# Optimization experiments

Hardware: AMD Instinct MI355X
Metric: run time of the kernel (lower is better)

## Reference

```python
import jax, jax.numpy as jnp
import numpy as np

B, I, T = 8192, 128, 21
H1, H2, H3 = 256, 256, 128


def _init(key, shape, fan_in):
    # torch-style uniform(-1/sqrt(fan_in), 1/sqrt(fan_in))
    bound = 1.0 / np.sqrt(fan_in)
    return jax.random.uniform(key, shape, jnp.float32, -bound, bound)


def setup_inputs() -> dict:
    key = jax.random.key(0)
    ks = jax.random.split(key, 16)
    x = jax.random.normal(ks[0], (B, I, T), jnp.float32)
    d = {"x": x}
    # stacked LSTM weights (PyTorch layout: W_ih (4H, in), gate order i,f,g,o)
    d["W1_ih"] = _init(ks[1], (4 * H1, I), H1)
    d["b1_ih"] = _init(ks[2], (4 * H1,), H1)
    d["b1_hh"] = _init(ks[3], (4 * H1,), H1)
    d["W2_ih"] = _init(ks[4], (4 * H2, H1), H2)
    d["b2_ih"] = _init(ks[5], (4 * H2,), H2)
    d["b2_hh"] = _init(ks[6], (4 * H2,), H2)
    d["W3_ih"] = _init(ks[7], (4 * H3, H2), H3)
    d["b3_ih"] = _init(ks[8], (4 * H3,), H3)
    d["b3_hh"] = _init(ks[9], (4 * H3,), H3)
    d["fc1_w"] = _init(ks[10], (1, H3), H3)
    d["fc1_b"] = _init(ks[11], (1,), H3)
    d["fc2_w"] = _init(ks[12], (T, T), T)
    d["fc2_b"] = _init(ks[13], (T,), T)
    return d


def _lstm_cell_step(xt, W_ih, b_ih, b_hh):
    # single timestep with h0 = c0 = 0, so the W_hh @ h0 term vanishes
    gates = xt @ W_ih.T + (b_ih + b_hh)          # (B, 21, 4H)
    i, f, g, o = jnp.split(gates, 4, axis=-1)    # torch gate order i,f,g,o
    c = jax.nn.sigmoid(i) * jnp.tanh(g)          # f * c0 = 0
    return jax.nn.sigmoid(o) * jnp.tanh(c)


def reference(x, W1_ih, b1_ih, b1_hh, W2_ih, b2_ih, b2_hh,
              W3_ih, b3_ih, b3_hh, fc1_w, fc1_b, fc2_w, fc2_b):
    # fold the 21 independent single-step columns into the batch dim
    xt = jnp.transpose(x, (0, 2, 1))             # (B, 21, I)
    h1 = _lstm_cell_step(xt, W1_ih, b1_ih, b1_hh)   # (B, 21, H1)
    h2 = _lstm_cell_step(h1, W2_ih, b2_ih, b2_hh)   # (B, 21, H2)
    h3 = _lstm_cell_step(h2, W3_ih, b3_ih, b3_hh)   # (B, 21, H3)
    y = h3 @ fc1_w.T + fc1_b                     # (B, 21, 1)
    y = y[..., 0][:, None, :]                    # (B, 1, 21)  == x_torch
    out = y @ fc2_w.T + fc2_b                    # (B, 1, 21)
    return out
```

## Files before the change

### kernel.cpp

```cpp
#include <hip/hip_runtime.h>
#include <hip/hip_bf16.h>
#include <stdint.h>


typedef __attribute__((ext_vector_type(8))) short bf16x8;
typedef __attribute__((ext_vector_type(4))) float f32x4;

#define M_ROWS 172032
#define BATCH  8192

__device__ __forceinline__ float bf2f(unsigned short u) {
    union { unsigned int i; float f; } v; v.i = ((unsigned int)u) << 16; return v.f;
}
__device__ __forceinline__ unsigned short f2bf(float f) {
    union { float f; unsigned int i; } v; v.f = f;
    unsigned int r = v.i + 0x7fffu + ((v.i >> 16) & 1u);
    return (unsigned short)(r >> 16);
}

#define LOG2E  1.44269504f
#define LOG2E2 2.88539008f

__device__ __forceinline__ float lstm_h(float gi, float gg, float go) {
    gg = fminf(fmaxf(gg, -15.0f), 15.0f);
    float Eg = __builtin_amdgcn_exp2f(gg * LOG2E2);
    float Ei = __builtin_amdgcn_exp2f(-gi * LOG2E);
    float c  = (Eg - 1.0f) * __builtin_amdgcn_rcpf((Eg + 1.0f) * (1.0f + Ei));
    float Eo = __builtin_amdgcn_exp2f(-go * LOG2E);
    float c2 = c * c;
    float num = c * fmaf(c2, c2 + 105.0f, 945.0f);
    float den = fmaf(c2, fmaf(15.0f, c2, 420.0f), 945.0f);
    return num * __builtin_amdgcn_rcpf(den * (1.0f + Eo));
}

__device__ __forceinline__ void gload_lds16(const unsigned short* g, unsigned short* l) {
    __builtin_amdgcn_global_load_lds(
        (const __attribute__((address_space(1))) unsigned int*)g,
        (__attribute__((address_space(3))) unsigned int*)l,
        16, 0, 0);
}

__global__ __launch_bounds__(256) void k_convert(
    const float* __restrict__ src, unsigned short* __restrict__ dst, int n4)
{
    int i = blockIdx.x * 256 + threadIdx.x;
    if (i < n4) {
        float4 v = ((const float4*)src)[i];
        ushort4 o;
        o.x = f2bf(v.x); o.y = f2bf(v.y); o.z = f2bf(v.z); o.w = f2bf(v.w);
        ((ushort4*)dst)[i] = o;
    }
}

__global__ __launch_bounds__(256) void k_transpose(
    const float* __restrict__ x, unsigned short* __restrict__ xt)
{
    __shared__ unsigned short tile[128 * 22];
    const int b = blockIdx.x, tid = threadIdx.x;
    const float* xb = x + (size_t)b * 2688;
    for (int idx = tid; idx < 2688; idx += 256) {
        int i = idx / 21, t = idx - i * 21;
        tile[i * 22 + t] = f2bf(xb[idx]);
    }
    __syncthreads();
    unsigned short* xtb = xt + (size_t)b * 2688;
    for (int idx = tid; idx < 2688; idx += 256) {
        int t = idx >> 7, i = idx & 127;
        xtb[t * 128 + i] = tile[i * 22 + t];
    }
}

template<int K, int HG>
__global__ __launch_bounds__(256, 2) void k_gemm_act(
    const unsigned short* __restrict__ A,
    const unsigned short* __restrict__ W,
    const float* __restrict__ bih,
    const float* __restrict__ bhh,
    unsigned short* __restrict__ Hout)
{
    __shared__ __align__(16) unsigned short As[128 * 64];
    __shared__ __align__(16) unsigned short Ws[192 * 64];

    const int tid  = threadIdx.x;
    const int wave = tid >> 6;
    const int lane = tid & 63;
    const int wm = wave >> 1;
    const int wn = wave & 1;
    const int r0 = blockIdx.x * 128;
    const int c0 = blockIdx.y * 64;
    const int csel = lane & 15;

    const unsigned short* aptr[4];
#pragma unroll
    for (int i = 0; i < 4; ++i) {
        int q16 = (wave * 4 + i) * 64 + lane;
        int row = q16 >> 3, pslot = q16 & 7;
        int lslot = pslot ^ (row & 7);
        aptr[i] = A + (size_t)(r0 + row) * K + lslot * 8;
    }
    const unsigned short* wptr[6];
#pragma unroll
    for (int i = 0; i < 6; ++i) {
        int q16 = (wave * 6 + i) * 64 + lane;
        int lrow = q16 >> 3, pslot = q16 & 7;
        int lslot = pslot ^ (lrow & 7);
        int gate = lrow >> 6, n = lrow & 63;
        int gbase = (gate == 0) ? 0 : (gate + 1) * HG;
        wptr[i] = W + (size_t)(gbase + c0 + n) * K + lslot * 8;
    }

    float bias[3][2];
#pragma unroll
    for (int n = 0; n < 2; ++n) {
        int cloc = c0 + wn * 32 + n * 16 + csel;
        bias[0][n] = bih[cloc] + bhh[cloc];
        bias[1][n] = bih[2 * HG + cloc] + bhh[2 * HG + cloc];
        bias[2][n] = bih[3 * HG + cloc] + bhh[3 * HG + cloc];
    }

    f32x4 acc[3][4][2];
#pragma unroll
    for (int g = 0; g < 3; ++g)
#pragma unroll
        for (int m = 0; m < 4; ++m)
#pragma unroll
            for (int n = 0; n < 2; ++n)
                acc[g][m][n] = (f32x4){0.f, 0.f, 0.f, 0.f};

#pragma unroll
    for (int kk = 0; kk < K; kk += 64) {
        if (kk) __syncthreads();
#pragma unroll
        for (int i = 0; i < 4; ++i)
            gload_lds16(aptr[i] + kk, &As[(wave * 4 + i) * 512]);
#pragma unroll
        for (int i = 0; i < 6; ++i)
            gload_lds16(wptr[i] + kk, &Ws[(wave * 6 + i) * 512]);
        __syncthreads();

#pragma unroll
        for (int ks = 0; ks < 64; ks += 32) {
            bf16x8 af[4];
            bf16x8 bfr[3][2];
            const int rsel = lane & 15;
            const int slot = (ks >> 3) | (lane >> 4);
            const int soff = (slot ^ (rsel & 7)) * 8;
#pragma unroll
            for (int m = 0; m < 4; ++m)
                af[m] = *(const bf16x8*)&As[(wm * 64 + m * 16 + rsel) * 64 + soff];
#pragma unroll
            for (int g = 0; g < 3; ++g)
#pragma unroll
                for (int n = 0; n < 2; ++n)
                    bfr[g][n] = *(const bf16x8*)&Ws[(g * 64 + wn * 32 + n * 16 + rsel) * 64 + soff];
#pragma unroll
            for (int g = 0; g < 3; ++g)
#pragma unroll
                for (int m = 0; m < 4; ++m)
#pragma unroll
                    for (int n = 0; n < 2; ++n)
                        acc[g][m][n] = __builtin_amdgcn_mfma_f32_16x16x32_bf16(
                            af[m], bfr[g][n], acc[g][m][n], 0, 0, 0);
        }
    }

    const int quad = lane >> 4;
#pragma unroll
    for (int m = 0; m < 4; ++m) {
#pragma unroll
        for (int n = 0; n < 2; ++n) {
            int cloc = wn * 32 + n * 16 + csel;
            f32x4 vi = acc[0][m][n], vg = acc[1][m][n], vo = acc[2][m][n];
#pragma unroll
            for (int r = 0; r < 4; ++r) {
                int row = r0 + wm * 64 + m * 16 + quad * 4 + r;
                float h = lstm_h(vi[r] + bias[0][n], vg[r] + bias[1][n],
                                 vo[r] + bias[2][n]);
                Hout[(size_t)row * HG + c0 + cloc] = f2bf(h);
            }
        }
    }
}

#define FSTR 169
__global__ __launch_bounds__(256) void k_final(
    const unsigned short* __restrict__ h3,
    const float* __restrict__ fc1w,
    const float* __restrict__ fc1b,
    const float* __restrict__ fc2w,
    const float* __restrict__ fc2b,
    float* __restrict__ out)
{
    __shared__ unsigned short ht[128 * FSTR];
    __shared__ float fwl[128];
    __shared__ float yl[168];
    __shared__ float f2l[441];
    __shared__ float f2bl[21];

    const int tid = threadIdx.x;
    const int b0 = blockIdx.x * 8;

    if (tid < 128) fwl[tid] = fc1w[tid];
    for (int i = tid; i < 441; i += 256) f2l[i] = fc2w[i];
    if (tid < 21) f2bl[tid] = fc2b[tid];

    const unsigned int* hsrc = (const unsigned int*)(h3 + (size_t)b0 * 2688);
    for (int gi = tid; gi < 10752; gi += 256) {
        unsigned int v = hsrc[gi];
        int e = gi * 2;
        int task = e >> 7;
        int c = e & 127;
        ht[c * FSTR + task] = (unsigned short)(v & 0xffffu);
        ht[(c + 1) * FSTR + task] = (unsigned short)(v >> 16);
    }
    __syncthreads();

    const float f1b = fc1b[0];
    if (tid < 168) {
        float s = f1b;
#pragma unroll 8
        for (int c = 0; c < 128; ++c)
            s += fwl[c] * bf2f(ht[c * FSTR + tid]);
        yl[tid] = s;
    }
    __syncthreads();
    if (tid < 168) {
        int bloc = tid / 21;
        int tp = tid - bloc * 21;
        float s = f2bl[tp];
#pragma unroll
        for (int t = 0; t < 21; ++t)
            s += yl[bloc * 21 + t] * f2l[tp * 21 + t];
        out[(size_t)(b0 + bloc) * 21 + tp] = s;
    }
}

extern "C" void kernel_launch(void* const* d_in, const int* in_sizes, int n_in,
                              void* d_out, int out_size, void* d_ws, size_t ws_size,
                              hipStream_t stream)
{
    const float* x    = (const float*)d_in[0];
    const float* W1   = (const float*)d_in[1];
    const float* b1i  = (const float*)d_in[2];
    const float* b1h  = (const float*)d_in[3];
    const float* W2   = (const float*)d_in[4];
    const float* b2i  = (const float*)d_in[5];
    const float* b2h  = (const float*)d_in[6];
    const float* W3   = (const float*)d_in[7];
    const float* b3i  = (const float*)d_in[8];
    const float* b3h  = (const float*)d_in[9];
    const float* fc1w = (const float*)d_in[10];
    const float* fc1b = (const float*)d_in[11];
    const float* fc2w = (const float*)d_in[12];
    const float* fc2b = (const float*)d_in[13];
    float* out = (float*)d_out;

    unsigned short* Wc1 = (unsigned short*)d_ws;
    unsigned short* Wc2 = Wc1 + 131072;
    unsigned short* Wc3 = Wc2 + 262144;
    unsigned short* buf = Wc3 + 131072;

    int C = 1;
    while (C < 64 && 1048576 + (size_t)(M_ROWS / C) * 1536 > ws_size) C <<= 1;
    const int R  = M_ROWS / C;
    const int Bc = BATCH / C;

    unsigned short* xt = buf;
    unsigned short* h1 = xt + (size_t)R * 128;
    unsigned short* h2 = h1 + (size_t)R * 256;
    unsigned short* h3 = h2 + (size_t)R * 256;

    k_convert<<<128, 256, 0, stream>>>(W1, Wc1, 32768);
    k_convert<<<256, 256, 0, stream>>>(W2, Wc2, 65536);
    k_convert<<<128, 256, 0, stream>>>(W3, Wc3, 32768);

    for (int c = 0; c < C; ++c) {
        const float* xc = x + (size_t)c * Bc * 2688;
        k_transpose<<<Bc, 256, 0, stream>>>(xc, xt);
        k_gemm_act<128, 256><<<dim3(R / 128, 4), 256, 0, stream>>>(xt, Wc1, b1i, b1h, h1);
        k_gemm_act<256, 256><<<dim3(R / 128, 4), 256, 0, stream>>>(h1, Wc2, b2i, b2h, h2);
        k_gemm_act<256, 128><<<dim3(R / 128, 2), 256, 0, stream>>>(h2, Wc3, b3i, b3h, h3);
        k_final<<<Bc / 8, 256, 0, stream>>>(h3, fc1w, fc1b, fc2w, fc2b,
                                            out + (size_t)c * Bc * 21);
    }
}
```

Baseline: 406.2 us.

## Double-buffer GEMM K-tiles, vectorize transpose, and merge weight conversions

The GEMM+activation kernel now stages 32-wide K slices in two LDS buffers with a new swizzle, prefetching the next slice while MFMAs run on the current one, so global loads can overlap with compute. The transpose kernel reads float4 and writes packed 32-bit pairs to cut memory instruction count. The three weight-conversion launches are merged into one kernel to save launch overhead. The trade-off is more barriers (one per 32-wide K step) and smaller tiles per sync, which could offset the overlap.

```diff
diff --git a/kernel.cpp b/kernel.cpp
--- a/kernel.cpp
+++ b/kernel.cpp
@@ -40,16 +40,21 @@
         16, 0, 0);
 }
 
-__global__ __launch_bounds__(256) void k_convert(
-    const float* __restrict__ src, unsigned short* __restrict__ dst, int n4)
+__global__ __launch_bounds__(256) void k_convert3(
+    const float* __restrict__ W1, const float* __restrict__ W2,
+    const float* __restrict__ W3,
+    unsigned short* __restrict__ d1, unsigned short* __restrict__ d2,
+    unsigned short* __restrict__ d3)
 {
     int i = blockIdx.x * 256 + threadIdx.x;
-    if (i < n4) {
-        float4 v = ((const float4*)src)[i];
-        ushort4 o;
-        o.x = f2bf(v.x); o.y = f2bf(v.y); o.z = f2bf(v.z); o.w = f2bf(v.w);
-        ((ushort4*)dst)[i] = o;
-    }
+    const float* src; unsigned short* dst; int off;
+    if (i < 32768)      { src = W1; dst = d1; off = i; }
+    else if (i < 98304) { src = W2; dst = d2; off = i - 32768; }
+    else                { src = W3; dst = d3; off = i - 98304; }
+    float4 v = ((const float4*)src)[off];
+    ushort4 o;
+    o.x = f2bf(v.x); o.y = f2bf(v.y); o.z = f2bf(v.z); o.w = f2bf(v.w);
+    ((ushort4*)dst)[off] = o;
 }
 
 __global__ __launch_bounds__(256) void k_transpose(
@@ -57,16 +62,25 @@
 {
     __shared__ unsigned short tile[128 * 22];
     const int b = blockIdx.x, tid = threadIdx.x;
-    const float* xb = x + (size_t)b * 2688;
-    for (int idx = tid; idx < 2688; idx += 256) {
-        int i = idx / 21, t = idx - i * 21;
-        tile[i * 22 + t] = f2bf(xb[idx]);
+    const float4* xb4 = (const float4*)(x + (size_t)b * 2688);
+    for (int j = tid; j < 672; j += 256) {
+        float4 v = xb4[j];
+        int e = j * 4;
+        int ii = e / 21, tt = e - ii * 21;
+        float vv[4] = {v.x, v.y, v.z, v.w};
+#pragma unroll
+        for (int k = 0; k < 4; ++k) {
+            tile[ii * 22 + tt] = f2bf(vv[k]);
+            if (++tt == 21) { tt = 0; ++ii; }
+        }
     }
     __syncthreads();
-    unsigned short* xtb = xt + (size_t)b * 2688;
-    for (int idx = tid; idx < 2688; idx += 256) {
-        int t = idx >> 7, i = idx & 127;
-        xtb[t * 128 + i] = tile[i * 22 + t];
+    unsigned int* xtb = (unsigned int*)(xt + (size_t)b * 2688);
+    for (int idx = tid; idx < 1344; idx += 256) {
+        int t = idx >> 6, i2 = (idx & 63) * 2;
+        unsigned int lo = tile[i2 * 22 + t];
+        unsigned int hi = tile[(i2 + 1) * 22 + t];
+        xtb[t * 64 + (idx & 63)] = lo | (hi << 16);
     }
 }
 
@@ -78,8 +92,8 @@
     const float* __restrict__ bhh,
     unsigned short* __restrict__ Hout)
 {
-    __shared__ __align__(16) unsigned short As[128 * 64];
-    __shared__ __align__(16) unsigned short Ws[192 * 64];
+    __shared__ __align__(16) unsigned short As[2][128 * 32];
+    __shared__ __align__(16) unsigned short Ws[2][192 * 32];
 
     const int tid  = threadIdx.x;
     const int wave = tid >> 6;
@@ -90,22 +104,22 @@
     const int c0 = blockIdx.y * 64;
     const int csel = lane & 15;
 
-    const unsigned short* aptr[4];
-#pragma unroll
-    for (int i = 0; i < 4; ++i) {
-        int q16 = (wave * 4 + i) * 64 + lane;
-        int row = q16 >> 3, pslot = q16 & 7;
-        int lslot = pslot ^ (row & 7);
+    const unsigned short* aptr[2];
+#pragma unroll
+    for (int i = 0; i < 2; ++i) {
+        int c = wave * 2 + i;
+        int row = c * 16 + (lane >> 2);
+        int lslot = (lane & 3) ^ ((row >> 1) & 3);
         aptr[i] = A + (size_t)(r0 + row) * K + lslot * 8;
     }
-    const unsigned short* wptr[6];
-#pragma unroll
-    for (int i = 0; i < 6; ++i) {
-        int q16 = (wave * 6 + i) * 64 + lane;
-        int lrow = q16 >> 3, pslot = q16 & 7;
-        int lslot = pslot ^ (lrow & 7);
-        int gate = lrow >> 6, n = lrow & 63;
+    const unsigned short* wptr[3];
+#pragma unroll
+    for (int i = 0; i < 3; ++i) {
+        int c = wave * 3 + i;
+        int row = c * 16 + (lane >> 2);
+        int gate = row >> 6, n = row & 63;
         int gbase = (gate == 0) ? 0 : (gate + 1) * HG;
+        int lslot = (lane & 3) ^ ((row >> 1) & 3);
         wptr[i] = W + (size_t)(gbase + c0 + n) * K + lslot * 8;
     }
 
@@ -128,31 +142,43 @@
                 acc[g][m][n] = (f32x4){0.f, 0.f, 0.f, 0.f};
 
 #pragma unroll
-    for (int kk = 0; kk < K; kk += 64) {
-        if (kk) __syncthreads();
-#pragma unroll
-        for (int i = 0; i < 4; ++i)
-            gload_lds16(aptr[i] + kk, &As[(wave * 4 + i) * 512]);
-#pragma unroll
-        for (int i = 0; i < 6; ++i)
-            gload_lds16(wptr[i] + kk, &Ws[(wave * 6 + i) * 512]);
-        __syncthreads();
-
-#pragma unroll
-        for (int ks = 0; ks < 64; ks += 32) {
+    for (int i = 0; i < 2; ++i)
+        gload_lds16(aptr[i], &As[0][(wave * 2 + i) * 512]);
+#pragma unroll
+    for (int i = 0; i < 3; ++i)
+        gload_lds16(wptr[i], &Ws[0][(wave * 3 + i) * 512]);
+    __syncthreads();
+
+    int cur = 0;
+#pragma unroll
+    for (int kk = 0; kk < K; kk += 32) {
+        if (kk + 32 < K) {
+#pragma unroll
+            for (int i = 0; i < 2; ++i)
+                gload_lds16(aptr[i] + kk + 32, &As[cur ^ 1][(wave * 2 + i) * 512]);
+#pragma unroll
+            for (int i = 0; i < 3; ++i)
+                gload_lds16(wptr[i] + kk + 32, &Ws[cur ^ 1][(wave * 3 + i) * 512]);
+        }
+
+        {
             bf16x8 af[4];
             bf16x8 bfr[3][2];
-            const int rsel = lane & 15;
-            const int slot = (ks >> 3) | (lane >> 4);
-            const int soff = (slot ^ (rsel & 7)) * 8;
-#pragma unroll
-            for (int m = 0; m < 4; ++m)
-                af[m] = *(const bf16x8*)&As[(wm * 64 + m * 16 + rsel) * 64 + soff];
+            const int q = lane >> 4;
+#pragma unroll
+            for (int m = 0; m < 4; ++m) {
+                int row = wm * 64 + m * 16 + csel;
+                int p = q ^ ((row >> 1) & 3);
+                af[m] = *(const bf16x8*)&As[cur][row * 32 + p * 8];
+            }
 #pragma unroll
             for (int g = 0; g < 3; ++g)
 #pragma unroll
-                for (int n = 0; n < 2; ++n)
-                    bfr[g][n] = *(const bf16x8*)&Ws[(g * 64 + wn * 32 + n * 16 + rsel) * 64 + soff];
+                for (int n = 0; n < 2; ++n) {
+                    int row = g * 64 + wn * 32 + n * 16 + csel;
+                    int p = q ^ ((row >> 1) & 3);
+                    bfr[g][n] = *(const bf16x8*)&Ws[cur][row * 32 + p * 8];
+                }
 #pragma unroll
             for (int g = 0; g < 3; ++g)
 #pragma unroll
@@ -162,6 +188,8 @@
                         acc[g][m][n] = __builtin_amdgcn_mfma_f32_16x16x32_bf16(
                             af[m], bfr[g][n], acc[g][m][n], 0, 0, 0);
         }
+        __syncthreads();
+        cur ^= 1;
     }
 
     const int quad = lane >> 4;
@@ -270,9 +298,7 @@
     unsigned short* h2 = h1 + (size_t)R * 256;
     unsigned short* h3 = h2 + (size_t)R * 256;
 
-    k_convert<<<128, 256, 0, stream>>>(W1, Wc1, 32768);
-    k_convert<<<256, 256, 0, stream>>>(W2, Wc2, 65536);
-    k_convert<<<128, 256, 0, stream>>>(W3, Wc3, 32768);
+    k_convert3<<<512, 256, 0, stream>>>(W1, W2, W3, Wc1, Wc2, Wc3);
 
     for (int c = 0; c < C; ++c) {
         const float* xc = x + (size_t)c * Bc * 2688;
```

After: 415.9 us. 2.4% more time.
